# Optimization experiments

Hardware: AMD Instinct MI355X
Metric: run time of the kernel (lower is better)

The kernel has to match this reference:

```python
import jax, jax.numpy as jnp
import numpy as np

# Grid constants (must match fill_max of coordinate inputs)
B, T, Y, X = 2, 8, 128, 128
YO, XO = 2 * Y - 1, 2 * X - 1  # spconv transpose: (in-1)*2 - 2*1 + 3 = 2*in - 1
EPS = 1e-5


def setup_inputs() -> dict:
    key = jax.random.key(0)
    ks = jax.random.split(key, 8)
    N, CIN, COUT = 262144, 128, 64
    feats = jax.random.normal(ks[0], (N, CIN), dtype=jnp.float32)
    # kernel-offset-major weight layout [kt, ky, kx, Cin, Cout]
    weight = jax.random.normal(ks[1], (3, 3, 3, CIN, COUT), dtype=jnp.float32) * 0.05
    gamma = jnp.ones((COUT,), jnp.float32)
    beta = jnp.zeros((COUT,), jnp.float32)
    coords_b = jax.random.randint(ks[2], (N,), 0, B, dtype=jnp.int32)
    coords_t = jax.random.randint(ks[3], (N,), 0, T, dtype=jnp.int32)
    coords_y = jax.random.randint(ks[4], (N,), 0, Y, dtype=jnp.int32)
    coords_x = jax.random.randint(ks[5], (N,), 0, X, dtype=jnp.int32)
    return {"feats": feats, "weight": weight, "gamma": gamma, "beta": beta,
            "coords_b": coords_b, "coords_t": coords_t,
            "coords_y": coords_y, "coords_x": coords_x}


def _sparse_deconv(feats, weight, cb, ct, cy, cx):
    """Rulebook-style transpose conv: for each of 27 kernel offsets,
    GEMM the input features and scatter-add into the (dense) output grid.
    Output coord: out = in*stride - pad + k. Grid padded by 1 so out-of-range
    contributions land in the halo and are sliced away (equivalent to spconv
    dropping rules outside the output extent)."""
    COUT = weight.shape[-1]
    grid = jnp.zeros((B, T + 2, YO + 2, XO + 2, COUT), feats.dtype)
    cnt = jnp.zeros((B, T + 2, YO + 2, XO + 2), jnp.float32)
    ones = jnp.ones((feats.shape[0],), jnp.float32)
    for kt in range(3):
        ot = ct - 1 + kt + 1  # stride 1 in t; +1 = halo offset
        for ky in range(3):
            oy = 2 * cy - 1 + ky + 1
            for kx in range(3):
                ox = 2 * cx - 1 + kx + 1
                msg = feats @ weight[kt, ky, kx]  # [N, Cout]
                grid = grid.at[cb, ot, oy, ox].add(msg)
                cnt = cnt.at[cb, ot, oy, ox].add(ones)
    return grid[:, 1:-1, 1:-1, 1:-1], cnt[:, 1:-1, 1:-1, 1:-1]


def reference(feats, weight, gamma, beta, coords_b, coords_t, coords_y, coords_x):
    # sort_sparse_tensor only reorders voxels; math is order-invariant here.
    grid, cnt = _sparse_deconv(feats, weight, coords_b, coords_t, coords_y, coords_x)
    mask = (cnt > 0).astype(grid.dtype)  # active output sites [B,T,YO,XO]
    n = jnp.maximum(mask.sum(), 1.0)
    # BatchNorm1d over active-site features (grid is exactly 0 at inactive sites)
    mean = grid.sum(axis=(0, 1, 2, 3)) / n
    var = (grid * grid).sum(axis=(0, 1, 2, 3)) / n - mean * mean  # biased var
    rstd = jax.lax.rsqrt(var + EPS)
    out = (grid - mean) * (rstd * gamma) + beta
    out = out * mask[..., None]  # keep inactive sites at zero (sparse semantics)
    return jax.nn.relu(out)
```

## Files before the change

### kernel.cpp

```cpp
#include <hip/hip_runtime.h>
#include <hip/hip_bf16.h>

#define BB   2
#define TT   8
#define YY   128
#define XX   128
#define CINv 128
#define COUTv 64
#define YOv  255
#define XOv  255
#define NVOX 262144
#define NSITES (BB*TT*YY*XX)
#define CAP  16
#define OUT_SITES (BB*TT*YOv*XOv)
#define OUT_ELEMS ((size_t)OUT_SITES*COUTv)

typedef float  f32x4  __attribute__((ext_vector_type(4)));
typedef __bf16 bf16x8 __attribute__((ext_vector_type(8)));
typedef unsigned int u32x4 __attribute__((ext_vector_type(4)));

union FragU { u32x4 u; bf16x8 b; };
union Pack8 { unsigned short s[8]; u32x4 u; };

constexpr size_t OFF_STATS = 0;
constexpr size_t OFF_CNT   = 1024;
constexpr size_t ZERO_BYTES= OFF_CNT + 1048576;
constexpr size_t OFF_DBF   = ZERO_BYTES;
constexpr size_t OFF_PB    = OFF_DBF + 67108864;
constexpr size_t OFF_MASK  = OFF_PB + 442368;
constexpr size_t OFF_SS    = OFF_MASK + 1048576;
constexpr size_t OFF_IDX   = OFF_SS + 1024;
constexpr size_t OFF_OUTB  = OFF_IDX;

__device__ __forceinline__ unsigned short f2bf(float f) {
    unsigned u = __float_as_uint(f);
    u += 0x7fffu + ((u >> 16) & 1u);
    return (unsigned short)(u >> 16);
}

__device__ __forceinline__ void gld16(const void* g, void* l) {
    __builtin_amdgcn_global_load_lds(
        (const __attribute__((address_space(1))) unsigned int*)g,
        (__attribute__((address_space(3))) unsigned int*)l, 16, 0, 0);
}

__global__ __launch_bounds__(256) void k_count(
    const int* __restrict__ cb, const int* __restrict__ ct,
    const int* __restrict__ cy, const int* __restrict__ cx,
    unsigned int* __restrict__ cnt, int* __restrict__ idx)
{
    int n = blockIdx.x * 256 + threadIdx.x;
    int site = ((cb[n] * TT + ct[n]) * YY + cy[n]) * XX + cx[n];
    unsigned slot = atomicAdd(cnt + site, 1u);
    if (slot < CAP) idx[site * CAP + slot] = n;
}

__global__ __launch_bounds__(256) void k_gather(
    const float* __restrict__ feats,
    const unsigned int* __restrict__ cnt, const int* __restrict__ idx,
    unsigned short* __restrict__ Dbf)
{
    int tid = blockIdx.x * 256 + threadIdx.x;
    int site = tid >> 4;
    int c8 = (tid & 15) * 8;
    unsigned c = cnt[site]; if (c > CAP) c = CAP;
    float a[8] = {0.f,0.f,0.f,0.f,0.f,0.f,0.f,0.f};
    const int* ip = idx + (size_t)site * CAP;
    for (unsigned v = 0; v < c; ++v) {
        int n = ip[v];
        const float4 f0 = *(const float4*)(feats + (size_t)n * CINv + c8);
        const float4 f1 = *(const float4*)(feats + (size_t)n * CINv + c8 + 4);
        a[0] += f0.x; a[1] += f0.y; a[2] += f0.z; a[3] += f0.w;
        a[4] += f1.x; a[5] += f1.y; a[6] += f1.z; a[7] += f1.w;
    }
    Pack8 p;
    #pragma unroll
    for (int j = 0; j < 8; ++j) p.s[j] = f2bf(a[j]);
    *(u32x4*)(Dbf + (size_t)site * CINv + c8) = p.u;
}

__global__ __launch_bounds__(64) void k_pack(
    const float* __restrict__ W, unsigned short* __restrict__ PB)
{
    int f = blockIdx.x;
    int w  = f >> 4;
    int kc = (f >> 2) & 3;
    int nt = f & 3;
    int lane = threadIdx.x;
    int q = lane >> 4, col = lane & 15;
    Pack8 p;
    #pragma unroll
    for (int j = 0; j < 8; ++j) {
        int k  = kc * 32 + q * 8 + j;
        int nn = nt * 16 + col;
        p.s[j] = f2bf(W[((size_t)w * CINv + k) * COUTv + nn]);
    }
    *(u32x4*)(PB + ((size_t)f * 64 + lane) * 8) = p.u;
}

__global__ __launch_bounds__(256) void k_mask(
    const unsigned int* __restrict__ occ,
    unsigned char* __restrict__ mask, unsigned int* __restrict__ ncnt)
{
    int s = blockIdx.x * 256 + threadIdx.x;
    bool found = false;
    if (s < OUT_SITES) {
        int xo = s % XOv; int r = s / XOv;
        int yo = r % YOv; r /= YOv;
        int to = r & 7;   int b = r >> 3;
        int cts[3]; int ntc = 0;
        for (int kt = 0; kt < 3; ++kt) { int c = to + 1 - kt; if (c >= 0 && c < TT) cts[ntc++] = c; }
        int cys[2]; int nyc;
        if (yo & 1) { cys[0] = (yo + 1) >> 1; cys[1] = (yo - 1) >> 1; nyc = 2; }
        else        { cys[0] = yo >> 1; nyc = 1; }
        int cxs[2]; int nxc;
        if (xo & 1) { cxs[0] = (xo + 1) >> 1; cxs[1] = (xo - 1) >> 1; nxc = 2; }
        else        { cxs[0] = xo >> 1; nxc = 1; }
        for (int i = 0; i < ntc && !found; ++i)
            for (int j = 0; j < nyc && !found; ++j)
                for (int k = 0; k < nxc && !found; ++k)
                    if (occ[((b * TT + cts[i]) * YY + cys[j]) * XX + cxs[k]]) found = true;
        mask[s] = found ? 1 : 0;
    }
    unsigned long long bal = __ballot(found);
    if ((threadIdx.x & 63) == 0) {
        unsigned c = (unsigned)__popcll(bal);
        if (c) atomicAdd(ncnt, c);
    }
}


#define BPASS(bt, A_a, A_b, SLOT) do {                                                   \
    _Pragma("unroll")                                                                    \
    for (int kc = 0; kc < 4; ++kc) {                                                     \
        FragU Bf[4];                                                                     \
        _Pragma("unroll")                                                                \
        for (int nt = 0; nt < 4; ++nt)                                                   \
            Bf[nt].u = *(const u32x4*)((bt) + (size_t)((kc * 4 + nt) * 64 + lane) * 8);  \
        _Pragma("unroll")                                                                \
        for (int nt = 0; nt < 4; ++nt) {                                                 \
            acc[SLOT][nt]     = __builtin_amdgcn_mfma_f32_16x16x32_bf16(                 \
                                    A_a[kc].b, Bf[nt].b, acc[SLOT][nt], 0, 0, 0);        \
            acc[SLOT + 2][nt] = __builtin_amdgcn_mfma_f32_16x16x32_bf16(                 \
                                    A_b[kc].b, Bf[nt].b, acc[SLOT + 2][nt], 0, 0, 0);    \
        }                                                                                \
    } } while (0)

__global__ __launch_bounds__(256, 3) void k_conv(
    const unsigned short* __restrict__ Dbf,
    const unsigned short* __restrict__ PB,
    unsigned short* __restrict__ outb,
    float* __restrict__ gsum, float* __restrict__ gsq)
{
    const int lane = threadIdx.x & 63;
    const int wave = threadIdx.x >> 6;
    const int bid = blockIdx.x;
    const int row_id = (bid & 7) * 510 + (bid >> 3);
    const int yo = row_id % YOv;
    int r2 = row_id / YOv;
    const int to = r2 & 7;
    const int b  = r2 >> 3;
    const int m = lane & 15, q = lane >> 4;

    __shared__ __align__(16) unsigned short shB[3 * 16 * 64 * 8];
    __shared__ float shsum[64], shsq[64];
    if (threadIdx.x < 64) { shsum[threadIdx.x] = 0.f; shsq[threadIdx.x] = 0.f; }

    int ycy[2], yky[2], ny;
    if ((yo & 1) == 0) { ny = 1; ycy[0] = yo >> 1; yky[0] = 1; }
    else { ny = 2; ycy[0] = (yo + 1) >> 1; yky[0] = 0; ycy[1] = (yo - 1) >> 1; yky[1] = 2; }

    f32x4 acc[4][4];
    #pragma unroll
    for (int ch = 0; ch < 4; ++ch)
        #pragma unroll
        for (int nt = 0; nt < 4; ++nt) acc[ch][nt] = (f32x4){0.f, 0.f, 0.f, 0.f};

    for (int kt = 0; kt < 3; ++kt) {
        int ct = to + 1 - kt;
        if (ct < 0 || ct >= TT) continue;
        for (int iy = 0; iy < ny; ++iy) {
            __syncthreads();
            {
                const char* gsrc = (const char*)PB + (size_t)((kt * 3 + yky[iy]) * 3) * 16384;
                char* ldst = (char*)shB;
                #pragma unroll
                for (int r = 0; r < 12; ++r)
                    gld16(gsrc + r * 4096 + threadIdx.x * 16,
                          ldst + r * 4096 + wave * 1024);
            }
            size_t plane = ((size_t)((b * TT + ct) * YY + ycy[iy])) * XX;
            const unsigned short* Ara0 = Dbf + (plane + (size_t)(2 * wave * 16 + m)) * CINv;
            const unsigned short* Arb0 = Dbf + (plane + (size_t)((2 * wave + 1) * 16 + m)) * CINv;
            FragU Aa[4], Ab[4];
            #pragma unroll
            for (int kc = 0; kc < 4; ++kc) {
                Aa[kc].u = *(const u32x4*)(Ara0 + kc * 32 + q * 8);
                Ab[kc].u = *(const u32x4*)(Arb0 + kc * 32 + q * 8);
            }
            __syncthreads();

            BPASS(shB + 8192,  Aa, Ab, 0);
            BPASS(shB + 16384, Aa, Ab, 1);

            {
                int cxb1 = (2 * wave + 1) * 16 + m + 1; if (cxb1 > 127) cxb1 = 127;
                const unsigned short* Ara1 = Dbf + (plane + (size_t)(2 * wave * 16 + m + 1)) * CINv;
                const unsigned short* Arb1 = Dbf + (plane + (size_t)cxb1) * CINv;
                #pragma unroll
                for (int kc = 0; kc < 4; ++kc) {
                    Aa[kc].u = *(const u32x4*)(Ara1 + kc * 32 + q * 8);
                    Ab[kc].u = *(const u32x4*)(Arb1 + kc * 32 + q * 8);
                }
            }
            BPASS(shB + 0, Aa, Ab, 1);
        }
    }

    size_t rowbase = ((size_t)((b * TT + to) * YOv + yo)) * XOv;
    float sl[4] = {0.f,0.f,0.f,0.f}, sq[4] = {0.f,0.f,0.f,0.f};
    #pragma unroll
    for (int ch = 0; ch < 4; ++ch) {
        int cb8 = 2 * wave + (ch >> 1);
        int px = ch & 1;
        #pragma unroll
        for (int nt = 0; nt < 4; ++nt) {
            int c = nt * 16 + m;
            #pragma unroll
            for (int i = 0; i < 4; ++i) {
                int r = q * 4 + i;
                int xo = 2 * (cb8 * 16 + r) + px;
                if (xo < XOv) {
                    float v = acc[ch][nt][i];
                    outb[(rowbase + xo) * COUTv + c] = f2bf(v);
                    sl[nt] += v; sq[nt] += v * v;
                }
            }
        }
    }
    #pragma unroll
    for (int nt = 0; nt < 4; ++nt) {
        sl[nt] += __shfl_xor(sl[nt], 16); sl[nt] += __shfl_xor(sl[nt], 32);
        sq[nt] += __shfl_xor(sq[nt], 16); sq[nt] += __shfl_xor(sq[nt], 32);
    }
    if (lane < 16) {
        #pragma unroll
        for (int nt = 0; nt < 4; ++nt) {
            atomicAdd(&shsum[nt * 16 + lane], sl[nt]);
            atomicAdd(&shsq [nt * 16 + lane], sq[nt]);
        }
    }
    __syncthreads();
    if (threadIdx.x < 64) {
        unsafeAtomicAdd(&gsum[threadIdx.x], shsum[threadIdx.x]);
        unsafeAtomicAdd(&gsq [threadIdx.x], shsq [threadIdx.x]);
    }
}

__global__ __launch_bounds__(64) void k_final(
    const float* __restrict__ gsum, const float* __restrict__ gsq,
    const unsigned int* __restrict__ ncnt,
    const float* __restrict__ gamma, const float* __restrict__ beta,
    float* __restrict__ scale, float* __restrict__ shift)
{
    int c = threadIdx.x;
    float nf = (float)max(*ncnt, 1u);
    float mean = gsum[c] / nf;
    float var  = gsq[c] / nf - mean * mean;
    float rstd = rsqrtf(var + 1e-5f);
    float sc = rstd * gamma[c];
    scale[c] = sc;
    shift[c] = beta[c] - mean * sc;
}

__global__ __launch_bounds__(256) void k_norm(
    const unsigned short* __restrict__ outb, float* __restrict__ out,
    const unsigned char* __restrict__ mask,
    const float* __restrict__ scale, const float* __restrict__ shift)
{
    __shared__ float ssc[64], ssh[64];
    if (threadIdx.x < 64) { ssc[threadIdx.x] = scale[threadIdx.x]; ssh[threadIdx.x] = shift[threadIdx.x]; }
    __syncthreads();
    size_t t = (size_t)blockIdx.x * 256 + threadIdx.x;
    size_t e = t * 8;
    if (e >= OUT_ELEMS) return;
    Pack8 p; p.u = *(const u32x4*)(outb + e);
    int c = (int)(e & 63);
    size_t site = e >> 6;
    float4 v0, v1;
    if (mask[site]) {
        float w[8];
        #pragma unroll
        for (int j = 0; j < 8; ++j) {
            float f = __uint_as_float((unsigned)p.s[j] << 16);
            w[j] = fmaxf(fmaf(f, ssc[c + j], ssh[c + j]), 0.f);
        }
        v0 = make_float4(w[0], w[1], w[2], w[3]);
        v1 = make_float4(w[4], w[5], w[6], w[7]);
    } else {
        v0 = make_float4(0.f, 0.f, 0.f, 0.f);
        v1 = v0;
    }
    *(float4*)(out + e) = v0;
    *(float4*)(out + e + 4) = v1;
}

extern "C" void kernel_launch(void* const* d_in, const int* in_sizes, int n_in,
                              void* d_out, int out_size, void* d_ws, size_t ws_size,
                              hipStream_t stream)
{
    const float* feats = (const float*)d_in[0];
    const float* W     = (const float*)d_in[1];
    const float* gamma = (const float*)d_in[2];
    const float* beta  = (const float*)d_in[3];
    const int* cb = (const int*)d_in[4];
    const int* ct = (const int*)d_in[5];
    const int* cy = (const int*)d_in[6];
    const int* cx = (const int*)d_in[7];
    float* out = (float*)d_out;

    char* ws = (char*)d_ws;
    float*          gsum = (float*)(ws + OFF_STATS);
    float*          gsq  = gsum + 64;
    unsigned int*   ncnt = (unsigned int*)(ws + OFF_STATS + 512);
    unsigned int*   cnt  = (unsigned int*)(ws + OFF_CNT);
    unsigned short* Dbf  = (unsigned short*)(ws + OFF_DBF);
    unsigned short* PB   = (unsigned short*)(ws + OFF_PB);
    unsigned char*  mask = (unsigned char*)(ws + OFF_MASK);
    float*          scale= (float*)(ws + OFF_SS);
    float*          shift= scale + 64;
    int*            idx  = (int*)(ws + OFF_IDX);
    unsigned short* outb = (unsigned short*)(ws + OFF_OUTB);

    hipMemsetAsync(d_ws, 0, ZERO_BYTES, stream);

    k_count<<<NVOX / 256, 256, 0, stream>>>(cb, ct, cy, cx, cnt, idx);
    k_gather<<<NSITES * 16 / 256, 256, 0, stream>>>(feats, cnt, idx, Dbf);
    k_pack<<<27 * 16, 64, 0, stream>>>(W, PB);
    k_mask<<<(OUT_SITES + 255) / 256, 256, 0, stream>>>(cnt, mask, ncnt);
    k_conv<<<BB * TT * YOv, 256, 0, stream>>>(Dbf, PB, outb, gsum, gsq);
    k_final<<<1, 64, 0, stream>>>(gsum, gsq, ncnt, gamma, beta, scale, shift);
    k_norm<<<(int)((OUT_ELEMS / 8 + 255) / 256), 256, 0, stream>>>(outb, out, mask, scale, shift);
}
```

Baseline: 864.2 us.

## Compute two output rows per block to reuse staged weight tiles

Each conv block now handles two output rows of the same parity (yo and yo+2). Those rows share the same kernel-offset weight slices, so each weight tile staged in LDS feeds twice as many MFMAs. The grid shrinks to 2048 blocks and accumulators double, which raises register pressure, so launch bounds drop from 3 to 2 blocks per CU. The last odd row (253) is handled alone through the has2 flag.

```diff
diff --git a/kernel.cpp b/kernel.cpp
--- a/kernel.cpp
+++ b/kernel.cpp
@@ -130,7 +130,9 @@
 }
 
 
-#define BPASS(bt, A_a, A_b, SLOT) do {                                                   \
+#define MFMA_BF16(A, B, C) __builtin_amdgcn_mfma_f32_16x16x32_bf16((A), (B), (C), 0, 0, 0)
+
+#define BPASS2(bt, SLOT) do {                                                            \
     _Pragma("unroll")                                                                    \
     for (int kc = 0; kc < 4; ++kc) {                                                     \
         FragU Bf[4];                                                                     \
@@ -139,14 +141,14 @@
             Bf[nt].u = *(const u32x4*)((bt) + (size_t)((kc * 4 + nt) * 64 + lane) * 8);  \
         _Pragma("unroll")                                                                \
         for (int nt = 0; nt < 4; ++nt) {                                                 \
-            acc[SLOT][nt]     = __builtin_amdgcn_mfma_f32_16x16x32_bf16(                 \
-                                    A_a[kc].b, Bf[nt].b, acc[SLOT][nt], 0, 0, 0);        \
-            acc[SLOT + 2][nt] = __builtin_amdgcn_mfma_f32_16x16x32_bf16(                 \
-                                    A_b[kc].b, Bf[nt].b, acc[SLOT + 2][nt], 0, 0, 0);    \
+            acc0[SLOT][nt]     = MFMA_BF16(Aa0[kc].b, Bf[nt].b, acc0[SLOT][nt]);         \
+            acc0[SLOT + 2][nt] = MFMA_BF16(Ab0[kc].b, Bf[nt].b, acc0[SLOT + 2][nt]);     \
+            acc1[SLOT][nt]     = MFMA_BF16(Aa1[kc].b, Bf[nt].b, acc1[SLOT][nt]);         \
+            acc1[SLOT + 2][nt] = MFMA_BF16(Ab1[kc].b, Bf[nt].b, acc1[SLOT + 2][nt]);     \
         }                                                                                \
     } } while (0)
 
-__global__ __launch_bounds__(256, 3) void k_conv(
+__global__ __launch_bounds__(256, 2) void k_conv(
     const unsigned short* __restrict__ Dbf,
     const unsigned short* __restrict__ PB,
     unsigned short* __restrict__ outb,
@@ -155,11 +157,17 @@
     const int lane = threadIdx.x & 63;
     const int wave = threadIdx.x >> 6;
     const int bid = blockIdx.x;
-    const int row_id = (bid & 7) * 510 + (bid >> 3);
-    const int yo = row_id % YOv;
-    int r2 = row_id / YOv;
+    const int row_id = (bid & 7) * 256 + (bid >> 3);
+    const int g  = row_id & 127;
+    int r2 = row_id >> 7;
     const int to = r2 & 7;
     const int b  = r2 >> 3;
+
+    int yo0; bool has2;
+    if (g < 64)       { yo0 = 4 * g;            has2 = true;  }
+    else if (g < 127) { yo0 = 4 * (g - 64) + 1; has2 = true;  }
+    else              { yo0 = 253;              has2 = false; }
+
     const int m = lane & 15, q = lane >> 4;
 
     __shared__ __align__(16) unsigned short shB[3 * 16 * 64 * 8];
@@ -167,14 +175,17 @@
     if (threadIdx.x < 64) { shsum[threadIdx.x] = 0.f; shsq[threadIdx.x] = 0.f; }
 
     int ycy[2], yky[2], ny;
-    if ((yo & 1) == 0) { ny = 1; ycy[0] = yo >> 1; yky[0] = 1; }
-    else { ny = 2; ycy[0] = (yo + 1) >> 1; yky[0] = 0; ycy[1] = (yo - 1) >> 1; yky[1] = 2; }
-
-    f32x4 acc[4][4];
+    if ((yo0 & 1) == 0) { ny = 1; ycy[0] = yo0 >> 1; yky[0] = 1; }
+    else { ny = 2; ycy[0] = (yo0 + 1) >> 1; yky[0] = 0; ycy[1] = (yo0 - 1) >> 1; yky[1] = 2; }
+
+    f32x4 acc0[4][4], acc1[4][4];
     #pragma unroll
     for (int ch = 0; ch < 4; ++ch)
         #pragma unroll
-        for (int nt = 0; nt < 4; ++nt) acc[ch][nt] = (f32x4){0.f, 0.f, 0.f, 0.f};
+        for (int nt = 0; nt < 4; ++nt) {
+            acc0[ch][nt] = (f32x4){0.f, 0.f, 0.f, 0.f};
+            acc1[ch][nt] = (f32x4){0.f, 0.f, 0.f, 0.f};
+        }
 
     for (int kt = 0; kt < 3; ++kt) {
         int ct = to + 1 - kt;
@@ -189,51 +200,88 @@
                     gld16(gsrc + r * 4096 + threadIdx.x * 16,
                           ldst + r * 4096 + wave * 1024);
             }
-            size_t plane = ((size_t)((b * TT + ct) * YY + ycy[iy])) * XX;
-            const unsigned short* Ara0 = Dbf + (plane + (size_t)(2 * wave * 16 + m)) * CINv;
-            const unsigned short* Arb0 = Dbf + (plane + (size_t)((2 * wave + 1) * 16 + m)) * CINv;
-            FragU Aa[4], Ab[4];
-            #pragma unroll
-            for (int kc = 0; kc < 4; ++kc) {
-                Aa[kc].u = *(const u32x4*)(Ara0 + kc * 32 + q * 8);
-                Ab[kc].u = *(const u32x4*)(Arb0 + kc * 32 + q * 8);
+            int cy0 = ycy[iy];
+            int cy1 = has2 ? cy0 + 1 : cy0;
+            size_t plane0 = ((size_t)((b * TT + ct) * YY + cy0)) * XX;
+            size_t plane1 = ((size_t)((b * TT + ct) * YY + cy1)) * XX;
+            FragU Aa0[4], Ab0[4], Aa1[4], Ab1[4];
+            {
+                const unsigned short* pa0 = Dbf + (plane0 + (size_t)(2 * wave * 16 + m)) * CINv;
+                const unsigned short* pb0 = Dbf + (plane0 + (size_t)((2 * wave + 1) * 16 + m)) * CINv;
+                const unsigned short* pa1 = Dbf + (plane1 + (size_t)(2 * wave * 16 + m)) * CINv;
+                const unsigned short* pb1 = Dbf + (plane1 + (size_t)((2 * wave + 1) * 16 + m)) * CINv;
+                #pragma unroll
+                for (int kc = 0; kc < 4; ++kc) {
+                    Aa0[kc].u = *(const u32x4*)(pa0 + kc * 32 + q * 8);
+                    Ab0[kc].u = *(const u32x4*)(pb0 + kc * 32 + q * 8);
+                    Aa1[kc].u = *(const u32x4*)(pa1 + kc * 32 + q * 8);
+                    Ab1[kc].u = *(const u32x4*)(pb1 + kc * 32 + q * 8);
+                }
             }
             __syncthreads();
 
-            BPASS(shB + 8192,  Aa, Ab, 0);
-            BPASS(shB + 16384, Aa, Ab, 1);
+            BPASS2(shB + 8192,  0);
+            BPASS2(shB + 16384, 1);
 
             {
                 int cxb1 = (2 * wave + 1) * 16 + m + 1; if (cxb1 > 127) cxb1 = 127;
-                const unsigned short* Ara1 = Dbf + (plane + (size_t)(2 * wave * 16 + m + 1)) * CINv;
-                const unsigned short* Arb1 = Dbf + (plane + (size_t)cxb1) * CINv;
+                const unsigned short* pa0 = Dbf + (plane0 + (size_t)(2 * wave * 16 + m + 1)) * CINv;
+                const unsigned short* pb0 = Dbf + (plane0 + (size_t)cxb1) * CINv;
+                const unsigned short* pa1 = Dbf + (plane1 + (size_t)(2 * wave * 16 + m + 1)) * CINv;
+                const unsigned short* pb1 = Dbf + (plane1 + (size_t)cxb1) * CINv;
                 #pragma unroll
                 for (int kc = 0; kc < 4; ++kc) {
-                    Aa[kc].u = *(const u32x4*)(Ara1 + kc * 32 + q * 8);
-                    Ab[kc].u = *(const u32x4*)(Arb1 + kc * 32 + q * 8);
+                    Aa0[kc].u = *(const u32x4*)(pa0 + kc * 32 + q * 8);
+                    Ab0[kc].u = *(const u32x4*)(pb0 + kc * 32 + q * 8);
+                    Aa1[kc].u = *(const u32x4*)(pa1 + kc * 32 + q * 8);
+                    Ab1[kc].u = *(const u32x4*)(pb1 + kc * 32 + q * 8);
                 }
             }
-            BPASS(shB + 0, Aa, Ab, 1);
-        }
-    }
-
-    size_t rowbase = ((size_t)((b * TT + to) * YOv + yo)) * XOv;
+            BPASS2(shB + 0, 1);
+        }
+    }
+
     float sl[4] = {0.f,0.f,0.f,0.f}, sq[4] = {0.f,0.f,0.f,0.f};
-    #pragma unroll
-    for (int ch = 0; ch < 4; ++ch) {
-        int cb8 = 2 * wave + (ch >> 1);
-        int px = ch & 1;
-        #pragma unroll
-        for (int nt = 0; nt < 4; ++nt) {
-            int c = nt * 16 + m;
+    {
+        size_t rowbase = ((size_t)((b * TT + to) * YOv + yo0)) * XOv;
+        #pragma unroll
+        for (int ch = 0; ch < 4; ++ch) {
+            int cb8 = 2 * wave + (ch >> 1);
+            int px = ch & 1;
             #pragma unroll
-            for (int i = 0; i < 4; ++i) {
-                int r = q * 4 + i;
-                int xo = 2 * (cb8 * 16 + r) + px;
-                if (xo < XOv) {
-                    float v = acc[ch][nt][i];
-                    outb[(rowbase + xo) * COUTv + c] = f2bf(v);
-                    sl[nt] += v; sq[nt] += v * v;
+            for (int nt = 0; nt < 4; ++nt) {
+                int c = nt * 16 + m;
+                #pragma unroll
+                for (int i = 0; i < 4; ++i) {
+                    int r = q * 4 + i;
+                    int xo = 2 * (cb8 * 16 + r) + px;
+                    if (xo < XOv) {
+                        float v = acc0[ch][nt][i];
+                        outb[(rowbase + xo) * COUTv + c] = f2bf(v);
+                        sl[nt] += v; sq[nt] += v * v;
+                    }
+                }
+            }
+        }
+    }
+    if (has2) {
+        size_t rowbase = ((size_t)((b * TT + to) * YOv + (yo0 + 2))) * XOv;
+        #pragma unroll
+        for (int ch = 0; ch < 4; ++ch) {
+            int cb8 = 2 * wave + (ch >> 1);
+            int px = ch & 1;
+            #pragma unroll
+            for (int nt = 0; nt < 4; ++nt) {
+                int c = nt * 16 + m;
+                #pragma unroll
+                for (int i = 0; i < 4; ++i) {
+                    int r = q * 4 + i;
+                    int xo = 2 * (cb8 * 16 + r) + px;
+                    if (xo < XOv) {
+                        float v = acc1[ch][nt][i];
+                        outb[(rowbase + xo) * COUTv + c] = f2bf(v);
+                        sl[nt] += v; sq[nt] += v * v;
+                    }
                 }
             }
         }
@@ -338,7 +386,7 @@
     k_gather<<<NSITES * 16 / 256, 256, 0, stream>>>(feats, cnt, idx, Dbf);
     k_pack<<<27 * 16, 64, 0, stream>>>(W, PB);
     k_mask<<<(OUT_SITES + 255) / 256, 256, 0, stream>>>(cnt, mask, ncnt);
-    k_conv<<<BB * TT * YOv, 256, 0, stream>>>(Dbf, PB, outb, gsum, gsq);
+    k_conv<<<2048, 256, 0, stream>>>(Dbf, PB, outb, gsum, gsq);
     k_final<<<1, 64, 0, stream>>>(gsum, gsq, ncnt, gamma, beta, scale, shift);
     k_norm<<<(int)((OUT_ELEMS / 8 + 255) / 256), 256, 0, stream>>>(outb, out, mask, scale, shift);
 }
```

Measured after the change: 826.5 us. -4.4%, faster.
